# Kernel tuning notes

Hardware: AMD Instinct MI355X
Metric: run time of the kernel (lower is better)

Reference implementation:

```python
import jax, jax.numpy as jnp
import numpy as np

B, L, D, H = 2, 1024, 768, 12
d = D // H  # attention_dim = 64

def setup_inputs() -> dict:
    key = jax.random.key(0)
    ks = jax.random.split(key, 8)
    s = 0.02
    return {
        "hidden_states": jax.random.normal(ks[0], (B, L, D), jnp.float32),
        "attention_mask": jnp.zeros((B, 1, 1, L), jnp.float32),
        "relative_attentions": jax.random.normal(ks[1], (B, L, L, d), jnp.float32),
        "Wq": jax.random.normal(ks[2], (D, D), jnp.float32) * s,
        "Wk": jax.random.normal(ks[3], (D, D), jnp.float32) * s,
        "Wv": jax.random.normal(ks[4], (D, D), jnp.float32) * s,
        "bv": jnp.zeros((D,), jnp.float32),
        "Wo": jax.random.normal(ks[5], (D, D), jnp.float32) * s,
        "bo": jnp.zeros((D,), jnp.float32),
    }

def reference(hidden_states, attention_mask, relative_attentions, Wq, Wk, Wv, bv, Wo, bo):
    # Linear weights stored [out, in] as in torch; y = x @ W.T
    q = hidden_states @ Wq.T
    k = hidden_states @ Wk.T
    v = hidden_states @ Wv.T + bv
    # F.linear(q, Wk.T) == q @ Wk ; F.linear(k, Wq.T) == k @ Wq
    rq = q @ Wk
    rk = k @ Wq
    split = lambda x: x.reshape(B, L, H, d).transpose(0, 2, 1, 3)  # [B,H,L,d]
    q, k, v, rq, rk = map(split, (q, k, v, rq, rk))
    scores = (
        jnp.einsum('bhld,bhrd->bhlr', q, k)
        + jnp.einsum('bhld,blrd->bhlr', rq, relative_attentions)
        + jnp.einsum('bhrd,blrd->bhlr', rk, relative_attentions)
    )
    scores = scores / jnp.sqrt(jnp.float32(3 * d)) + attention_mask
    probs = jax.nn.softmax(scores, axis=-1)  # dropout omitted (eval mode)
    attended = jnp.einsum('bhlr,bhrd->blhd', probs, v).reshape(B, L, D)
    return attended @ Wo.T + bo
```

## Files before the change

kernel.cpp:

```cpp
#include <hip/hip_runtime.h>
#include <hip/hip_bf16.h>

typedef unsigned short u16;
typedef __attribute__((ext_vector_type(8))) __bf16 bf16x8;
typedef __attribute__((ext_vector_type(4))) float f32x4;

#define BB 2
#define LL 1024
#define DD 768
#define HH 12

__device__ __forceinline__ u16 f2b(float v) {
  unsigned u = __builtin_bit_cast(unsigned, v);
  return (u16)((u + 0x7fffu + ((u >> 16) & 1u)) >> 16);
}

__global__ void k_cast(const float* __restrict__ in, u16* __restrict__ out, int n) {
  int i = blockIdx.x * blockDim.x + threadIdx.x;
  if (i < n) out[i] = f2b(in[i]);
}

__global__ __launch_bounds__(256) void k_gemm_nt(
    const u16* __restrict__ A, int lda, long long sAb, long long sAh,
    const u16* __restrict__ Bt, int ldb, long long sBb, long long sBh,
    float* __restrict__ Cf, u16* __restrict__ Cb, int ldc, long long sCb, long long sCh,
    const float* __restrict__ bias, int M, int N, int K, int nInner)
{
  __shared__ __align__(16) u16 As[64][40];
  __shared__ __align__(16) u16 Bs[64][40];
  int z = blockIdx.z, zb = z / nInner, zh = z - zb * nInner;
  A  += zb * sAb + zh * sAh;
  Bt += zb * sBb + zh * sBh;
  long long coff = zb * sCb + zh * sCh;
  int m0 = blockIdx.y * 64, n0 = blockIdx.x * 64;
  int tid = threadIdx.x, lane = tid & 63, w = tid >> 6;
  int wm = (w >> 1) * 32, wn = (w & 1) * 32;
  int arow = tid >> 2, acol = (tid & 3) * 8;
  int frow = lane & 15, kf = (lane >> 4) * 8;
  f32x4 acc[2][2] = {};
  for (int k0 = 0; k0 < K; k0 += 32) {
    *(uint4*)&As[arow][acol] = *(const uint4*)&A[(size_t)(m0 + arow) * lda + k0 + acol];
    *(uint4*)&Bs[arow][acol] = *(const uint4*)&Bt[(size_t)(n0 + arow) * ldb + k0 + acol];
    __syncthreads();
    bf16x8 af0 = *(const bf16x8*)&As[wm + frow][kf];
    bf16x8 af1 = *(const bf16x8*)&As[wm + 16 + frow][kf];
    bf16x8 bg0 = *(const bf16x8*)&Bs[wn + frow][kf];
    bf16x8 bg1 = *(const bf16x8*)&Bs[wn + 16 + frow][kf];
    acc[0][0] = __builtin_amdgcn_mfma_f32_16x16x32_bf16(af0, bg0, acc[0][0], 0, 0, 0);
    acc[0][1] = __builtin_amdgcn_mfma_f32_16x16x32_bf16(af0, bg1, acc[0][1], 0, 0, 0);
    acc[1][0] = __builtin_amdgcn_mfma_f32_16x16x32_bf16(af1, bg0, acc[1][0], 0, 0, 0);
    acc[1][1] = __builtin_amdgcn_mfma_f32_16x16x32_bf16(af1, bg1, acc[1][1], 0, 0, 0);
    __syncthreads();
  }
  int cr = (lane >> 4) * 4, cc = lane & 15;
  for (int mi = 0; mi < 2; mi++)
    for (int ni = 0; ni < 2; ni++) {
      int col = n0 + wn + ni * 16 + cc;
      float bval = bias ? bias[col] : 0.f;
      #pragma unroll
      for (int j = 0; j < 4; j++) {
        int row = m0 + wm + mi * 16 + cr + j;
        float v = acc[mi][ni][j] + bval;
        size_t idx = (size_t)coff + (size_t)row * ldc + col;
        if (Cf) Cf[idx] = v;
        if (Cb) Cb[idx] = f2b(v);
      }
    }
}

__global__ __launch_bounds__(256) void k_gemm_nn(
    const u16* __restrict__ A, int lda, long long sAb, long long sAh,
    const u16* __restrict__ Bm, int ldb, long long sBb, long long sBh,
    float* __restrict__ Cf, u16* __restrict__ Cb, int ldc, long long sCb, long long sCh,
    const float* __restrict__ bias, int M, int N, int K, int nInner)
{
  __shared__ __align__(16) u16 As[64][40];
  __shared__ __align__(16) u16 Bs[64][40];
  int z = blockIdx.z, zb = z / nInner, zh = z - zb * nInner;
  A  += zb * sAb + zh * sAh;
  Bm += zb * sBb + zh * sBh;
  long long coff = zb * sCb + zh * sCh;
  int m0 = blockIdx.y * 64, n0 = blockIdx.x * 64;
  int tid = threadIdx.x, lane = tid & 63, w = tid >> 6;
  int wm = (w >> 1) * 32, wn = (w & 1) * 32;
  int arow = tid >> 2, acol = (tid & 3) * 8;
  int brow = tid >> 3, bcol = (tid & 7) * 8;
  int frow = lane & 15, kf = (lane >> 4) * 8;
  f32x4 acc[2][2] = {};
  for (int k0 = 0; k0 < K; k0 += 32) {
    *(uint4*)&As[arow][acol] = *(const uint4*)&A[(size_t)(m0 + arow) * lda + k0 + acol];
    union { uint4 v; u16 s[8]; } t4;
    t4.v = *(const uint4*)&Bm[(size_t)(k0 + brow) * ldb + n0 + bcol];
    #pragma unroll
    for (int j = 0; j < 8; j++) Bs[bcol + j][brow] = t4.s[j];
    __syncthreads();
    bf16x8 af0 = *(const bf16x8*)&As[wm + frow][kf];
    bf16x8 af1 = *(const bf16x8*)&As[wm + 16 + frow][kf];
    bf16x8 bg0 = *(const bf16x8*)&Bs[wn + frow][kf];
    bf16x8 bg1 = *(const bf16x8*)&Bs[wn + 16 + frow][kf];
    acc[0][0] = __builtin_amdgcn_mfma_f32_16x16x32_bf16(af0, bg0, acc[0][0], 0, 0, 0);
    acc[0][1] = __builtin_amdgcn_mfma_f32_16x16x32_bf16(af0, bg1, acc[0][1], 0, 0, 0);
    acc[1][0] = __builtin_amdgcn_mfma_f32_16x16x32_bf16(af1, bg0, acc[1][0], 0, 0, 0);
    acc[1][1] = __builtin_amdgcn_mfma_f32_16x16x32_bf16(af1, bg1, acc[1][1], 0, 0, 0);
    __syncthreads();
  }
  int cr = (lane >> 4) * 4, cc = lane & 15;
  for (int mi = 0; mi < 2; mi++)
    for (int ni = 0; ni < 2; ni++) {
      int col = n0 + wn + ni * 16 + cc;
      float bval = bias ? bias[col] : 0.f;
      #pragma unroll
      for (int j = 0; j < 4; j++) {
        int row = m0 + wm + mi * 16 + cr + j;
        float v = acc[mi][ni][j] + bval;
        size_t idx = (size_t)coff + (size_t)row * ldc + col;
        if (Cf) Cf[idx] = v;
        if (Cb) Cb[idx] = f2b(v);
      }
    }
}

__global__ __launch_bounds__(256) void k_relterms(
    const float* __restrict__ rel, const float* __restrict__ rqf,
    const float* __restrict__ rkf, float* __restrict__ scores)
{
  __shared__ __align__(16) float rqs[8][776];
  int blk = blockIdx.x;
  int rc = blk & 7;
  int t  = blk >> 3;
  int b  = t >> 7;
  int l0 = (t & 127) << 3;
  int tid = threadIdx.x;
  #pragma unroll
  for (int j = 0; j < 6; j++) {
    int i = j * 256 + tid;
    int rr = i / 192, cc = (i - rr * 192) * 4;
    *(float4*)&rqs[rr][cc] = *(const float4*)&rqf[((size_t)b * LL + l0 + rr) * DD + cc];
  }
  __syncthreads();
  int g = tid >> 5, tr = tid & 31;
  int l = l0 + g;
  const float4* rq4 = (const float4*)&rqs[g][0];
  #pragma unroll
  for (int rt = 0; rt < 2; rt++) {
    int r0 = rc * 128 + rt * 64 + tr;
    const float4* rel0 = (const float4*)(rel + (((size_t)b * LL + l) * LL + r0) * 64);
    const float4* rel1 = rel0 + 512;
    const float4* rk0 = (const float4*)(rkf + ((size_t)b * LL + r0) * DD);
    const float4* rk1 = rk0 + 6144;
    float s0[12], s1[12];
    #pragma unroll
    for (int h = 0; h < 12; h++) { s0[h] = 0.f; s1[h] = 0.f; }
    for (int db = 0; db < 16; db++) {
      float4 v0 = rel0[db], v1 = rel1[db];
      #pragma unroll
      for (int h = 0; h < 12; h++) {
        float4 a = rq4[h * 16 + db];
        float4 p = rk0[h * 16 + db];
        float4 q = rk1[h * 16 + db];
        s0[h] += v0.x * (a.x + p.x) + v0.y * (a.y + p.y) + v0.z * (a.z + p.z) + v0.w * (a.w + p.w);
        s1[h] += v1.x * (a.x + q.x) + v1.y * (a.y + q.y) + v1.z * (a.z + q.z) + v1.w * (a.w + q.w);
      }
    }
    #pragma unroll
    for (int h = 0; h < 12; h++) {
      size_t idx = ((size_t)(b * HH + h) * LL + l) * LL + r0;
      scores[idx] += s0[h];
      scores[idx + 32] += s1[h];
    }
  }
}

__global__ __launch_bounds__(256) void k_softmax(float* __restrict__ scores,
                                                 const float* __restrict__ mask)
{
  __shared__ float red[4];
  int z = blockIdx.x;
  int b = z / (HH * LL);
  float* row = scores + (size_t)z * LL;
  int tid = threadIdx.x;
  const float inv = 0.07216878364870322f;
  float4 x = ((const float4*)row)[tid];
  float4 mk = ((const float4*)(mask + (size_t)b * LL))[tid];
  x.x = x.x * inv + mk.x; x.y = x.y * inv + mk.y;
  x.z = x.z * inv + mk.z; x.w = x.w * inv + mk.w;
  float m = fmaxf(fmaxf(x.x, x.y), fmaxf(x.z, x.w));
  for (int i = 1; i < 64; i <<= 1) m = fmaxf(m, __shfl_xor(m, i));
  if ((tid & 63) == 0) red[tid >> 6] = m;
  __syncthreads();
  m = fmaxf(fmaxf(red[0], red[1]), fmaxf(red[2], red[3]));
  float e0 = expf(x.x - m), e1 = expf(x.y - m), e2 = expf(x.z - m), e3 = expf(x.w - m);
  float s = e0 + e1 + e2 + e3;
  for (int i = 1; i < 64; i <<= 1) s += __shfl_xor(s, i);
  __syncthreads();
  if ((tid & 63) == 0) red[tid >> 6] = s;
  __syncthreads();
  float rs = 1.f / (red[0] + red[1] + red[2] + red[3]);
  u16* prow = (u16*)row;
  ushort4 o;
  o.x = f2b(e0 * rs); o.y = f2b(e1 * rs); o.z = f2b(e2 * rs); o.w = f2b(e3 * rs);
  ((ushort4*)prow)[tid] = o;
}

extern "C" void kernel_launch(void* const* d_in, const int* in_sizes, int n_in,
                              void* d_out, int out_size, void* d_ws, size_t ws_size,
                              hipStream_t stream)
{
  const float* hs   = (const float*)d_in[0];
  const float* mask = (const float*)d_in[1];
  const float* rel  = (const float*)d_in[2];
  const float* Wq   = (const float*)d_in[3];
  const float* Wk   = (const float*)d_in[4];
  const float* Wv   = (const float*)d_in[5];
  const float* bv   = (const float*)d_in[6];
  const float* Wo   = (const float*)d_in[7];
  const float* bo   = (const float*)d_in[8];
  float* out = (float*)d_out;

  size_t o = 0;
  char* wsb = (char*)d_ws;
  auto alc = [&](size_t bytes) { void* p = wsb + o; o += (bytes + 255) & ~(size_t)255; return p; };
  u16* hs_bf = (u16*)alc(2048ull * 768 * 2);
  u16* wq_bf = (u16*)alc(768ull * 768 * 2);
  u16* wk_bf = (u16*)alc(768ull * 768 * 2);
  u16* wv_bf = (u16*)alc(768ull * 768 * 2);
  u16* wo_bf = (u16*)alc(768ull * 768 * 2);
  u16* q_bf  = (u16*)alc(2048ull * 768 * 2);
  u16* k_bf  = (u16*)alc(2048ull * 768 * 2);
  u16* v_bf  = (u16*)alc(2048ull * 768 * 2);
  float* rq_f = (float*)alc(2048ull * 768 * 4);
  float* rk_f = (float*)alc(2048ull * 768 * 4);
  u16* att_bf = (u16*)alc(2048ull * 768 * 2);
  float* scores = (float*)alc((size_t)BB * HH * LL * LL * 4);
  (void)ws_size; (void)in_sizes; (void)n_in; (void)out_size;

  k_cast<<<dim3((1572864 + 255) / 256), dim3(256), 0, stream>>>(hs, hs_bf, 1572864);
  k_cast<<<dim3((589824 + 255) / 256), dim3(256), 0, stream>>>(Wq, wq_bf, 589824);
  k_cast<<<dim3((589824 + 255) / 256), dim3(256), 0, stream>>>(Wk, wk_bf, 589824);
  k_cast<<<dim3((589824 + 255) / 256), dim3(256), 0, stream>>>(Wv, wv_bf, 589824);
  k_cast<<<dim3((589824 + 255) / 256), dim3(256), 0, stream>>>(Wo, wo_bf, 589824);

  dim3 gP(768 / 64, 2048 / 64, 1);
  k_gemm_nt<<<gP, 256, 0, stream>>>(hs_bf, 768, 0, 0, wq_bf, 768, 0, 0,
                                    nullptr, q_bf, 768, 0, 0, nullptr, 2048, 768, 768, 1);
  k_gemm_nt<<<gP, 256, 0, stream>>>(hs_bf, 768, 0, 0, wk_bf, 768, 0, 0,
                                    nullptr, k_bf, 768, 0, 0, nullptr, 2048, 768, 768, 1);
  k_gemm_nt<<<gP, 256, 0, stream>>>(hs_bf, 768, 0, 0, wv_bf, 768, 0, 0,
                                    nullptr, v_bf, 768, 0, 0, bv, 2048, 768, 768, 1);
  k_gemm_nn<<<gP, 256, 0, stream>>>(q_bf, 768, 0, 0, wk_bf, 768, 0, 0,
                                    rq_f, nullptr, 768, 0, 0, nullptr, 2048, 768, 768, 1);
  k_gemm_nn<<<gP, 256, 0, stream>>>(k_bf, 768, 0, 0, wq_bf, 768, 0, 0,
                                    rk_f, nullptr, 768, 0, 0, nullptr, 2048, 768, 768, 1);

  dim3 gS(16, 16, 24);
  k_gemm_nt<<<gS, 256, 0, stream>>>(q_bf, 768, 786432LL, 64LL, k_bf, 768, 786432LL, 64LL,
                                    scores, nullptr, 1024, 12582912LL, 1048576LL,
                                    nullptr, 1024, 1024, 64, 12);
  k_relterms<<<dim3(2048), dim3(256), 0, stream>>>(rel, rq_f, rk_f, scores);
  k_softmax<<<dim3(BB * HH * LL), dim3(256), 0, stream>>>(scores, mask);
  dim3 gPV(1, 16, 24);
  k_gemm_nn<<<gPV, 256, 0, stream>>>((u16*)scores, 2048, 25165824LL, 2097152LL,
                                     v_bf, 768, 786432LL, 64LL,
                                     nullptr, att_bf, 768, 786432LL, 64LL,
                                     nullptr, 1024, 64, 1024, 12);
  k_gemm_nt<<<gP, 256, 0, stream>>>(att_bf, 768, 0, 0, wo_bf, 768, 0, 0,
                                    out, nullptr, 768, 0, 0, bo, 2048, 768, 768, 1);
}
```

Before: 1.817 ms.

## Stage relative-attention tile through LDS with coalesced loads and register prefetch

```diff
diff --git a/kernel.cpp b/kernel.cpp
--- a/kernel.cpp
+++ b/kernel.cpp
@@ -3,6 +3,7 @@
 
 typedef unsigned short u16;
 typedef __attribute__((ext_vector_type(8))) __bf16 bf16x8;
+typedef __attribute__((ext_vector_type(8))) unsigned short us8;
 typedef __attribute__((ext_vector_type(4))) float f32x4;
 
 #define BB 2
@@ -13,6 +14,9 @@
 __device__ __forceinline__ u16 f2b(float v) {
   unsigned u = __builtin_bit_cast(unsigned, v);
   return (u16)((u + 0x7fffu + ((u >> 16) & 1u)) >> 16);
+}
+__device__ __forceinline__ float b2f(u16 b) {
+  return __builtin_bit_cast(float, (unsigned)b << 16);
 }
 
 __global__ void k_cast(const float* __restrict__ in, u16* __restrict__ out, int n) {
@@ -124,49 +128,81 @@
     const float* __restrict__ rel, const float* __restrict__ rqf,
     const float* __restrict__ rkf, float* __restrict__ scores)
 {
-  __shared__ __align__(16) float rqs[8][776];
+  __shared__ __align__(16) float rqs[4][776];
+  __shared__ __align__(16) u16 rels[128][72];
   int blk = blockIdx.x;
   int rc = blk & 7;
   int t  = blk >> 3;
-  int b  = t >> 7;
-  int l0 = (t & 127) << 3;
+  int b  = t >> 8;
+  int l0 = (t & 255) << 2;
   int tid = threadIdx.x;
+  int ll = tid >> 6;
+  int u  = tid & 63;
+  int p  = tid & 1;
+  int rl = (tid >> 1) & 31;
+
   #pragma unroll
-  for (int j = 0; j < 6; j++) {
+  for (int j = 0; j < 3; j++) {
     int i = j * 256 + tid;
     int rr = i / 192, cc = (i - rr * 192) * 4;
     *(float4*)&rqs[rr][cc] = *(const float4*)&rqf[((size_t)b * LL + l0 + rr) * DD + cc];
   }
-  __syncthreads();
-  int g = tid >> 5, tr = tid & 31;
-  int l = l0 + g;
-  const float4* rq4 = (const float4*)&rqs[g][0];
+
+  const float4* relbase = (const float4*)(rel + (((size_t)b * LL + l0 + ll) * LL + rc * 128) * 64);
+  float4 st[8];
   #pragma unroll
-  for (int rt = 0; rt < 2; rt++) {
-    int r0 = rc * 128 + rt * 64 + tr;
-    const float4* rel0 = (const float4*)(rel + (((size_t)b * LL + l) * LL + r0) * 64);
-    const float4* rel1 = rel0 + 512;
-    const float4* rk0 = (const float4*)(rkf + ((size_t)b * LL + r0) * DD);
-    const float4* rk1 = rk0 + 6144;
-    float s0[12], s1[12];
-    #pragma unroll
-    for (int h = 0; h < 12; h++) { s0[h] = 0.f; s1[h] = 0.f; }
-    for (int db = 0; db < 16; db++) {
-      float4 v0 = rel0[db], v1 = rel1[db];
+  for (int j = 0; j < 8; j++) st[j] = relbase[u + j * 64];
+
+  const float4* rq4 = (const float4*)&rqs[ll][0];
+  float s[12];
+  #pragma unroll
+  for (int h = 0; h < 12; h++) s[h] = 0.f;
+
+  for (int c = 0; c < 4; c++) {
+    __syncthreads();
+    #pragma unroll
+    for (int j = 0; j < 8; j++) {
+      int f = u + j * 64;
+      int r = f >> 4, dg = f & 15;
+      ushort4 w4;
+      w4.x = f2b(st[j].x); w4.y = f2b(st[j].y); w4.z = f2b(st[j].z); w4.w = f2b(st[j].w);
+      *(ushort4*)&rels[ll * 32 + r][dg * 4] = w4;
+    }
+    __syncthreads();
+    if (c < 3) {
+      const float4* nxt = relbase + (size_t)(c + 1) * 512;
+      #pragma unroll
+      for (int j = 0; j < 8; j++) st[j] = nxt[u + j * 64];
+    }
+    int rg = rc * 128 + c * 32 + rl;
+    const float4* rk4 = (const float4*)(rkf + ((size_t)b * LL + rg) * DD);
+    const u16* relrow = &rels[ll * 32 + rl][0];
+    #pragma unroll
+    for (int h = 0; h < 12; h++) s[h] = 0.f;
+    #pragma unroll
+    for (int dgh = 0; dgh < 4; dgh++) {
+      us8 rv = *(const us8*)&relrow[p * 32 + dgh * 8];
+      float f0x = b2f(rv[0]), f0y = b2f(rv[1]), f0z = b2f(rv[2]), f0w = b2f(rv[3]);
+      float f1x = b2f(rv[4]), f1y = b2f(rv[5]), f1z = b2f(rv[6]), f1w = b2f(rv[7]);
+      int fo = p * 8 + dgh * 2;
       #pragma unroll
       for (int h = 0; h < 12; h++) {
-        float4 a = rq4[h * 16 + db];
-        float4 p = rk0[h * 16 + db];
-        float4 q = rk1[h * 16 + db];
-        s0[h] += v0.x * (a.x + p.x) + v0.y * (a.y + p.y) + v0.z * (a.z + p.z) + v0.w * (a.w + p.w);
-        s1[h] += v1.x * (a.x + q.x) + v1.y * (a.y + q.y) + v1.z * (a.z + q.z) + v1.w * (a.w + q.w);
+        float4 a0 = rq4[h * 16 + fo], a1 = rq4[h * 16 + fo + 1];
+        float4 k0 = rk4[h * 16 + fo], k1 = rk4[h * 16 + fo + 1];
+        s[h] += f0x * (a0.x + k0.x) + f0y * (a0.y + k0.y)
+              + f0z * (a0.z + k0.z) + f0w * (a0.w + k0.w)
+              + f1x * (a1.x + k1.x) + f1y * (a1.y + k1.y)
+              + f1z * (a1.z + k1.z) + f1w * (a1.w + k1.w);
       }
     }
+    int l = l0 + ll;
     #pragma unroll
     for (int h = 0; h < 12; h++) {
-      size_t idx = ((size_t)(b * HH + h) * LL + l) * LL + r0;
-      scores[idx] += s0[h];
-      scores[idx + 32] += s1[h];
+      float tot = s[h] + __shfl_xor(s[h], 1);
+      if (p == 0) {
+        size_t idx = ((size_t)(b * HH + h) * LL + l) * LL + rg;
+        scores[idx] += tot;
+      }
     }
   }
 }
@@ -256,7 +292,7 @@
   k_gemm_nt<<<gS, 256, 0, stream>>>(q_bf, 768, 786432LL, 64LL, k_bf, 768, 786432LL, 64LL,
                                     scores, nullptr, 1024, 12582912LL, 1048576LL,
                                     nullptr, 1024, 1024, 64, 12);
-  k_relterms<<<dim3(2048), dim3(256), 0, stream>>>(rel, rq_f, rk_f, scores);
+  k_relterms<<<dim3(4096), dim3(256), 0, stream>>>(rel, rq_f, rk_f, scores);
   k_softmax<<<dim3(BB * HH * LL), dim3(256), 0, stream>>>(scores, mask);
   dim3 gPV(1, 16, 24);
   k_gemm_nn<<<gPV, 256, 0, stream>>>((u16*)scores, 2048, 25165824LL, 2097152LL,
```

New measurement: 3.877 ms. +113.3%, slower.
